# Kernel tuning notes

Hardware: AMD Instinct MI355X
Metric: run time of the kernel (lower is better)

The kernel has to match this reference:

```python
import jax, jax.numpy as jnp
import numpy as np

NEG_INF_SCALE = -1e9


def setup_inputs() -> dict:
    key = jax.random.key(0)
    ks = jax.random.split(key, 8)
    B, T, M, D = 64, 1024, 256, 1024
    query = jax.random.normal(ks[0], (B, 1, M), dtype=jnp.float32)
    keys = jax.random.normal(ks[1], (B, T, M), dtype=jnp.float32)
    values = jax.random.normal(ks[2], (B, T, D), dtype=jnp.float32)
    mask = jax.random.randint(ks[3], (B, 1, T), 0, 2).astype(jnp.float32)
    # MLP params (scaled like torch default init ~ 1/sqrt(fan_in))
    W1 = jax.random.normal(ks[4], (4 * M, D), dtype=jnp.float32) / np.sqrt(4 * M)
    b1 = jnp.zeros((D,), dtype=jnp.float32)
    W2 = jax.random.normal(ks[5], (D, D), dtype=jnp.float32) / np.sqrt(D)
    b2 = jnp.zeros((D,), dtype=jnp.float32)
    w_score = jax.random.normal(ks[6], (D, 1), dtype=jnp.float32) / np.sqrt(D)
    b_score = jnp.zeros((1,), dtype=jnp.float32)
    return {"query": query, "keys": keys, "values": values, "mask": mask,
            "W1": W1, "b1": b1, "W2": W2, "b2": b2,
            "w_score": w_score, "b_score": b_score}


def reference(query, keys, values, mask, W1, b1, W2, b2, w_score, b_score):
    # query: [B,1,M] broadcast against keys: [B,T,M]
    q = jnp.broadcast_to(query, keys.shape)
    att_input = jnp.concatenate([q, keys, q - keys, q * keys], axis=-1)  # [B,T,4M]
    h = jax.nn.relu(att_input @ W1 + b1)   # [B,T,D]
    h = jax.nn.relu(h @ W2 + b2)           # [B,T,D]
    score = h @ w_score + b_score          # [B,T,1]
    logits = jnp.swapaxes(score, 1, 2)     # [B,1,T]
    logits = logits + mask * NEG_INF_SCALE
    attn = jax.nn.softmax(logits, axis=-1)  # [B,1,T]
    out = jnp.matmul(attn, values)          # [B,1,D]
    return out
```

## Files before the change

kernel.cpp:

```cpp
#include <hip/hip_runtime.h>

#define DEV __device__ __forceinline__

typedef __attribute__((ext_vector_type(4))) float f32x4;
typedef __attribute__((ext_vector_type(8))) short short8;
typedef __attribute__((ext_vector_type(4))) short s16x4;
typedef __attribute__((ext_vector_type(4))) float f32x4v;

DEV short f2bf(float f) {
  union { float f; unsigned u; } v; v.f = f;
  unsigned r = (v.u + 0x7FFFu + ((v.u >> 16) & 1u)) >> 16;
  return (short)r;
}

DEV void gload16(const void* g, void* l) {
  __builtin_amdgcn_global_load_lds(
      (const __attribute__((address_space(1))) void*)g,
      (__attribute__((address_space(3))) void*)l, 16, 0, 0);
}

#define BAR() __builtin_amdgcn_s_barrier()
#define LGKMW(n)                                              \
  {                                                           \
    asm volatile("s_waitcnt lgkmcnt(" #n ")" ::: "memory");   \
    __builtin_amdgcn_sched_barrier(0);                        \
  }
#define VMW(n)                                                \
  {                                                           \
    asm volatile("s_waitcnt vmcnt(" #n ")" ::: "memory");     \
    __builtin_amdgcn_sched_barrier(0);                        \
  }


__global__ __launch_bounds__(256) void k_prep_all(
    const float* __restrict__ keys, const float* __restrict__ w2,
    const float* __restrict__ w1, const float* __restrict__ query,
    const float* __restrict__ b1, short* __restrict__ keysb,
    short* __restrict__ w2f, short* __restrict__ wktf,
    float* __restrict__ biasb) {
  __shared__ __align__(16) char smem[45056];
  const int bid = blockIdx.x;
  const int tid = threadIdx.x;

  if (bid < 256) {
    short (*tile)[64][72] = (short (*)[64][72])(smem);
    float (*qlds)[256] = (float (*)[256])(smem + 36864);
    float (*redm)[64][4] = (float (*)[64][4])(smem + 40960);
    const int r = bid;
    const int bg = r & 15, d0g = r >> 4, d0 = d0g * 64;
    const int d = tid & 63, mq = tid >> 6;

    for (int idx = tid; idx < 1024; idx += 256)
      qlds[idx >> 8][idx & 255] = query[(bg * 4 + (idx >> 8)) * 256 + (idx & 255)];
    __syncthreads();

    float bacc[4] = {0.f, 0.f, 0.f, 0.f};
    const int l = tid & 63, cgl = tid >> 6;

    for (int mc = 0; mc < 4; ++mc) {
#pragma unroll 4
      for (int i = 0; i < 16; ++i) {
        int ml = i * 4 + mq;
        int m = mc * 64 + ml;
        float wa = w1[(size_t)m * 1024 + d0 + d];
        float wb = w1[(size_t)(256 + m) * 1024 + d0 + d];
        float wc = w1[(size_t)(512 + m) * 1024 + d0 + d];
        float wd = w1[(size_t)(768 + m) * 1024 + d0 + d];
        float bc = wb - wc, ac = wa + wc;
#pragma unroll
        for (int bb = 0; bb < 4; ++bb) {
          float qv = qlds[bb][m];
          tile[bb][d][ml] = f2bf(bc + qv * wd);
          bacc[bb] += qv * ac;
        }
      }
      __syncthreads();
#pragma unroll
      for (int bb = 0; bb < 4; ++bb) {
        short* ob = wktf + (size_t)(bg * 4 + bb) * 262144;
#pragma unroll
        for (int kh = 0; kh < 2; ++kh) {
          short8 v = *(const short8*)&tile[bb][cgl * 16 + (l & 15)]
                                          [kh * 32 + (l >> 4) * 8];
          *(short8*)&ob[((size_t)((mc * 2 + kh) * 64 + d0g * 4 + cgl)) * 512 + l * 8] = v;
        }
      }
      __syncthreads();
    }

    redm[0][d][mq] = bacc[0];
    redm[1][d][mq] = bacc[1];
    redm[2][d][mq] = bacc[2];
    redm[3][d][mq] = bacc[3];
    __syncthreads();
    const int bb = tid >> 6, dd = tid & 63;
    biasb[(bg * 4 + bb) * 1024 + d0 + dd] =
        redm[bb][dd][0] + redm[bb][dd][1] + redm[bb][dd][2] + redm[bb][dd][3] +
        b1[d0 + dd];
  } else if (bid < 512) {
    float (*tile)[65] = (float (*)[65])(smem);
    const int r = bid - 256;
    const int kt = r & 15, n0 = (r >> 4) * 64;
    const int a = tid & 63, q = tid >> 6;
#pragma unroll
    for (int i = 0; i < 16; ++i) {
      int kk = i * 4 + q;
      tile[kk][a] = w2[(size_t)(kt * 64 + kk) * 1024 + n0 + a];
    }
    __syncthreads();
    const int l = tid & 63, cgl = tid >> 6;
#pragma unroll
    for (int kh = 0; kh < 2; ++kh) {
      short8 v;
#pragma unroll
      for (int j = 0; j < 8; ++j)
        v[j] = f2bf(tile[kh * 32 + (l >> 4) * 8 + j][cgl * 16 + (l & 15)]);
      *(short8*)&w2f[((size_t)((kt * 2 + kh) * 64 + (n0 >> 4) + cgl)) * 512 + l * 8] = v;
    }
  } else {
    int i = ((bid - 512) * 256 + tid) * 8;
    f32x4v v0 = *(const f32x4v*)(keys + i);
    f32x4v v1 = *(const f32x4v*)(keys + i + 4);
    short8 s;
    s[0] = f2bf(v0[0]); s[1] = f2bf(v0[1]); s[2] = f2bf(v0[2]); s[3] = f2bf(v0[3]);
    s[4] = f2bf(v1[0]); s[5] = f2bf(v1[1]); s[6] = f2bf(v1[2]); s[7] = f2bf(v1[3]);
    *(short8*)(keysb + i) = s;
  }
}


template <int MODE>
__global__ __launch_bounds__(256, 2) void k_gemm(const short* __restrict__ A,
                                                 const short* __restrict__ Bf,
                                                 const float* __restrict__ bias,
                                                 const float* __restrict__ wscore,
                                                 short* __restrict__ hout,
                                                 float* __restrict__ spart) {
  __shared__ short lds[32768];
  constexpr int SK = (MODE == 1) ? 256 : 1024;
  constexpr int KT = (MODE == 1) ? 4 : 16;

  const int tid = threadIdx.x;
  const int bx = blockIdx.x;
  const int L = (bx & 7) * 256 + (bx >> 3);

  const short *Ab, *Bb;
  const float *biasp, *wsp = nullptr;
  short* houtp = nullptr;
  int rt, ct;
  if constexpr (MODE == 1) {
    const int b = L >> 5;
    rt = (L >> 2) & 7; ct = L & 3;
    Ab = A + ((size_t)(b * 1024 + rt * 128)) * 256;
    Bb = Bf + (size_t)b * 262144;
    biasp = bias + b * 1024 + ct * 256;
    houtp = hout + ((size_t)(b * 1024 + rt * 128)) * 1024 + ct * 256;
  } else {
    rt = L >> 2; ct = L & 3;
    Ab = A + (size_t)rt * 128 * 1024;
    Bb = Bf;
    biasp = bias + ct * 256;
    wsp = wscore + ct * 256;
  }

  int gA[4], dA[4];
#pragma unroll
  for (int j = 0; j < 4; ++j) {
    int s = tid + j * 256, row = s >> 3, kc = (s & 7) ^ (row & 7);
    gA[j] = row * SK + kc * 8;
    dA[j] = s * 8;
  }
  auto STAGE = [&](int kt) {
    const int bb = (kt & 3) * 8192;
#pragma unroll
    for (int j = 0; j < 4; ++j) gload16(Ab + gA[j] + kt * 64, &lds[bb + dA[j]]);
  };

  const int lane = tid & 63, l15 = lane & 15, l4 = lane >> 4, wc = tid >> 6;
  const int afo0 = l15 * 64 + ((l4 ^ (l15 & 7)) * 8);
  const int afo1 = l15 * 64 + (((4 + l4) ^ (l15 & 7)) * 8);

  f32x4 acc[8][4];
#pragma unroll
  for (int m = 0; m < 8; ++m)
#pragma unroll
    for (int n = 0; n < 4; ++n) acc[m][n] = f32x4{0.f, 0.f, 0.f, 0.f};
  short8 bf[2][4][2];
  short8 af[8];

#define LOADB(kt, BK_)                                                          \
  _Pragma("unroll") for (int n_ = 0; n_ < 4; ++n_) {                            \
    _Pragma("unroll") for (int kh_ = 0; kh_ < 2; ++kh_) {                       \
      bf[BK_][n_][kh_] = *(const short8*)(Bb +                                  \
          ((size_t)(((kt) * 2 + kh_) * 64 + ct * 16 + n_ * 4 + wc) << 9) +      \
          lane * 8);                                                            \
    }                                                                           \
  }

  STAGE(0); LOADB(0, 0);
  STAGE(1); LOADB(1, 1);
  VMW(12);
  BAR();

#pragma unroll
  for (int t = 0; t < KT; ++t) {
    const int bb = (t & 3) * 8192;
#pragma unroll
    for (int m = 0; m < 8; ++m) af[m] = *(const short8*)&lds[bb + afo0 + m * 1024];
    LGKMW(0);
    __builtin_amdgcn_s_setprio(1);
#pragma unroll
    for (int m = 0; m < 8; ++m)
#pragma unroll
      for (int n = 0; n < 4; ++n)
        acc[m][n] = __builtin_amdgcn_mfma_f32_16x16x32_bf16(bf[t & 1][n][0], af[m],
                                                            acc[m][n], 0, 0, 0);
    __builtin_amdgcn_s_setprio(0);
#pragma unroll
    for (int m = 0; m < 8; ++m) af[m] = *(const short8*)&lds[bb + afo1 + m * 1024];
    if (t + 2 < KT) STAGE(t + 2);
    LGKMW(0);
    __builtin_amdgcn_s_setprio(1);
#pragma unroll
    for (int m = 0; m < 8; ++m)
#pragma unroll
      for (int n = 0; n < 4; ++n)
        acc[m][n] = __builtin_amdgcn_mfma_f32_16x16x32_bf16(bf[t & 1][n][1], af[m],
                                                            acc[m][n], 0, 0, 0);
    __builtin_amdgcn_s_setprio(0);
    if (t + 2 < KT) {
      LOADB(t + 2, (t & 1));
      VMW(12);
    } else {
      VMW(0);
    }
    BAR();
  }
#undef LOADB

  if constexpr (MODE == 1) {
    float bv[4][4];
#pragma unroll
    for (int n = 0; n < 4; ++n)
#pragma unroll
      for (int r2 = 0; r2 < 4; ++r2)
        bv[n][r2] = biasp[n * 64 + wc * 16 + l4 * 4 + r2];
#pragma unroll
    for (int m = 0; m < 8; ++m) {
      int row = m * 16 + l15;
#pragma unroll
      for (int n = 0; n < 4; ++n) {
        s16x4 pk;
#pragma unroll
        for (int r2 = 0; r2 < 4; ++r2)
          pk[r2] = f2bf(fmaxf(acc[m][n][r2] + bv[n][r2], 0.f));
        *(s16x4*)&houtp[(size_t)row * 1024 + n * 64 + wc * 16 + l4 * 4] = pk;
      }
    }
  } else {
    float bv[4][4], wv[4][4];
#pragma unroll
    for (int n = 0; n < 4; ++n)
#pragma unroll
      for (int r2 = 0; r2 < 4; ++r2) {
        int c = n * 64 + wc * 16 + l4 * 4 + r2;
        bv[n][r2] = biasp[c];
        wv[n][r2] = wsp[c];
      }
    float* so = spart + ((size_t)(ct * 4 + wc) << 16) + rt * 128;
#pragma unroll
    for (int m = 0; m < 8; ++m) {
      float s = 0.f;
#pragma unroll
      for (int n = 0; n < 4; ++n)
#pragma unroll
        for (int r2 = 0; r2 < 4; ++r2)
          s += fmaxf(acc[m][n][r2] + bv[n][r2], 0.f) * wv[n][r2];
      s += __shfl_xor(s, 16);
      s += __shfl_xor(s, 32);
      if (lane < 16) so[m * 16 + l15] = s;
    }
  }
}

__global__ __launch_bounds__(256) void k_out(const float* __restrict__ spart,
                                             const float* __restrict__ mask,
                                             const float* __restrict__ bscore,
                                             const float* __restrict__ values,
                                             float* __restrict__ part) {
  const int b = blockIdx.x >> 3, ts = blockIdx.x & 7;
  const int tid = threadIdx.x;
  __shared__ float sm[1024];
  __shared__ float red[8];
  const float bs = bscore[0];
  float lmax = -3.0e38f;
  for (int t = tid; t < 1024; t += 256) {
    float s = bs;
#pragma unroll
    for (int c = 0; c < 16; ++c) s += spart[(size_t)c * 65536 + b * 1024 + t];
    float lg = s + mask[b * 1024 + t] * (-1e9f);
    sm[t] = lg;
    lmax = fmaxf(lmax, lg);
  }
  for (int o = 32; o; o >>= 1) lmax = fmaxf(lmax, __shfl_xor(lmax, o));
  const int wid = tid >> 6, lane = tid & 63;
  if (lane == 0) red[wid] = lmax;
  __syncthreads();
  float bmax = fmaxf(fmaxf(red[0], red[1]), fmaxf(red[2], red[3]));
  float lsum = 0.f;
  for (int t = tid; t < 1024; t += 256) {
    float e = __expf(sm[t] - bmax);
    sm[t] = e;
    lsum += e;
  }
  for (int o = 32; o; o >>= 1) lsum += __shfl_xor(lsum, o);
  __syncthreads();
  if (lane == 0) red[wid] = lsum;
  __syncthreads();
  const float inv = 1.0f / (red[0] + red[1] + red[2] + red[3]);

  const float* vb = values + ((size_t)b * 1024 + ts * 128) * 1024 + tid * 4;
  f32x4 acc = {0.f, 0.f, 0.f, 0.f};
#pragma unroll 8
  for (int t = 0; t < 128; ++t) {
    f32x4v v = *(const f32x4v*)(vb + (size_t)t * 1024);
    float a = sm[ts * 128 + t] * inv;
    acc[0] += a * v[0]; acc[1] += a * v[1]; acc[2] += a * v[2]; acc[3] += a * v[3];
  }
  *(f32x4*)(part + ((size_t)(b * 8 + ts)) * 1024 + tid * 4) = acc;
}

__global__ __launch_bounds__(256) void k_red(const float* __restrict__ part,
                                             float* __restrict__ out) {
  const int b = blockIdx.x;
  const int c4 = threadIdx.x * 4;
  f32x4 s = {0.f, 0.f, 0.f, 0.f};
#pragma unroll
  for (int ts = 0; ts < 8; ++ts) {
    f32x4v v = *(const f32x4v*)(part + ((size_t)(b * 8 + ts)) * 1024 + c4);
    s[0] += v[0]; s[1] += v[1]; s[2] += v[2]; s[3] += v[3];
  }
  *(f32x4*)(out + b * 1024 + c4) = s;
}


extern "C" void kernel_launch(void* const* d_in, const int* in_sizes, int n_in,
                              void* d_out, int out_size, void* d_ws, size_t ws_size,
                              hipStream_t stream) {
  const float* query  = (const float*)d_in[0];
  const float* keys   = (const float*)d_in[1];
  const float* values = (const float*)d_in[2];
  const float* mask   = (const float*)d_in[3];
  const float* W1     = (const float*)d_in[4];
  const float* b1     = (const float*)d_in[5];
  const float* W2     = (const float*)d_in[6];
  const float* b2     = (const float*)d_in[7];
  const float* wscore = (const float*)d_in[8];
  const float* bscore = (const float*)d_in[9];
  float* out = (float*)d_out;

  char* ws = (char*)d_ws;
  short* keysb = (short*)(ws);
  short* wktf  = (short*)(ws + 33554432ull);
  short* w2f   = (short*)(ws + 67108864ull);
  float* biasb = (float*)(ws + 69206016ull);
  short* h1    = (short*)(ws + 69468160ull);
  float* spart = (float*)(ws + 203685888ull);
  float* part  = (float*)(ws + 207880192ull);

  k_prep_all<<<8704, 256, 0, stream>>>(keys, W2, W1, query, b1,
                                       keysb, w2f, wktf, biasb);

  k_gemm<1><<<2048, 256, 0, stream>>>(keysb, wktf, biasb, nullptr, h1, nullptr);
  k_gemm<2><<<2048, 256, 0, stream>>>(h1, w2f, b2, wscore, nullptr, spart);

  k_out<<<512, 256, 0, stream>>>(spart, mask, bscore, values, part);
  k_red<<<64, 256, 0, stream>>>(part, out);
}
```

Measured before the change: 253.7 us.

## Halve GEMM row tile to 64 with 3-stage LDS ring and just-in-time B loads

Shrinks the per-block M tile from 128 to 64 rows, doubling the grid to 4096 blocks, and cuts LDS to a 3-buffer ring of 64x64 tiles so three blocks can share a CU. B fragments are now loaded from global right before each k-half instead of being prefetched two steps ahead, which lowers register pressure. The column mapping per wave changes so each wave owns a contiguous 64-column strip, and the epilogues are updated to match. Each B fragment is now reused across half as many rows, which raises B traffic and exposes more global-load latency in exchange for higher occupancy.

After: 269.6 us. +6.3%, slower.

```diff
diff --git a/kernel.cpp b/kernel.cpp
--- a/kernel.cpp
+++ b/kernel.cpp
@@ -130,107 +130,106 @@
 
 
 template <int MODE>
-__global__ __launch_bounds__(256, 2) void k_gemm(const short* __restrict__ A,
+__global__ __launch_bounds__(256, 3) void k_gemm(const short* __restrict__ A,
                                                  const short* __restrict__ Bf,
                                                  const float* __restrict__ bias,
                                                  const float* __restrict__ wscore,
                                                  short* __restrict__ hout,
                                                  float* __restrict__ spart) {
-  __shared__ short lds[32768];
+  __shared__ short lds[12288];
   constexpr int SK = (MODE == 1) ? 256 : 1024;
   constexpr int KT = (MODE == 1) ? 4 : 16;
 
   const int tid = threadIdx.x;
   const int bx = blockIdx.x;
-  const int L = (bx & 7) * 256 + (bx >> 3);
+  const int L = (bx & 7) * 512 + (bx >> 3);
 
   const short *Ab, *Bb;
   const float *biasp, *wsp = nullptr;
   short* houtp = nullptr;
   int rt, ct;
   if constexpr (MODE == 1) {
-    const int b = L >> 5;
-    rt = (L >> 2) & 7; ct = L & 3;
-    Ab = A + ((size_t)(b * 1024 + rt * 128)) * 256;
+    const int b = L >> 6;
+    rt = (L >> 2) & 15; ct = L & 3;
+    Ab = A + ((size_t)(b * 1024 + rt * 64)) * 256;
     Bb = Bf + (size_t)b * 262144;
     biasp = bias + b * 1024 + ct * 256;
-    houtp = hout + ((size_t)(b * 1024 + rt * 128)) * 1024 + ct * 256;
+    houtp = hout + ((size_t)(b * 1024 + rt * 64)) * 1024 + ct * 256;
   } else {
     rt = L >> 2; ct = L & 3;
-    Ab = A + (size_t)rt * 128 * 1024;
+    Ab = A + (size_t)rt * 64 * 1024;
     Bb = Bf;
     biasp = bias + ct * 256;
     wsp = wscore + ct * 256;
   }
 
-  int gA[4], dA[4];
-#pragma unroll
-  for (int j = 0; j < 4; ++j) {
+  int gA[2], dA[2];
+#pragma unroll
+  for (int j = 0; j < 2; ++j) {
     int s = tid + j * 256, row = s >> 3, kc = (s & 7) ^ (row & 7);
     gA[j] = row * SK + kc * 8;
     dA[j] = s * 8;
   }
   auto STAGE = [&](int kt) {
-    const int bb = (kt & 3) * 8192;
-#pragma unroll
-    for (int j = 0; j < 4; ++j) gload16(Ab + gA[j] + kt * 64, &lds[bb + dA[j]]);
+    const int bb = (kt % 3) * 4096;
+#pragma unroll
+    for (int j = 0; j < 2; ++j) gload16(Ab + gA[j] + kt * 64, &lds[bb + dA[j]]);
   };
 
   const int lane = tid & 63, l15 = lane & 15, l4 = lane >> 4, wc = tid >> 6;
   const int afo0 = l15 * 64 + ((l4 ^ (l15 & 7)) * 8);
   const int afo1 = l15 * 64 + (((4 + l4) ^ (l15 & 7)) * 8);
 
-  f32x4 acc[8][4];
-#pragma unroll
-  for (int m = 0; m < 8; ++m)
+  f32x4 acc[4][4];
+#pragma unroll
+  for (int m = 0; m < 4; ++m)
 #pragma unroll
     for (int n = 0; n < 4; ++n) acc[m][n] = f32x4{0.f, 0.f, 0.f, 0.f};
-  short8 bf[2][4][2];
-  short8 af[8];
-
-#define LOADB(kt, BK_)                                                          \
+  short8 bf[4];
+  short8 af[4];
+
+#define LOADB(kt, kh_)                                                          \
   _Pragma("unroll") for (int n_ = 0; n_ < 4; ++n_) {                            \
-    _Pragma("unroll") for (int kh_ = 0; kh_ < 2; ++kh_) {                       \
-      bf[BK_][n_][kh_] = *(const short8*)(Bb +                                  \
-          ((size_t)(((kt) * 2 + kh_) * 64 + ct * 16 + n_ * 4 + wc) << 9) +      \
-          lane * 8);                                                            \
-    }                                                                           \
-  }
-
-  STAGE(0); LOADB(0, 0);
-  STAGE(1); LOADB(1, 1);
-  VMW(12);
+    bf[n_] = *(const short8*)(Bb +                                              \
+        ((size_t)(((kt) * 2 + (kh_)) * 64 + ct * 16 + wc * 4 + n_) << 9) +      \
+        lane * 8);                                                              \
+  }
+
+  STAGE(0);
+  STAGE(1);
+  VMW(2);
   BAR();
 
 #pragma unroll
   for (int t = 0; t < KT; ++t) {
-    const int bb = (t & 3) * 8192;
-#pragma unroll
-    for (int m = 0; m < 8; ++m) af[m] = *(const short8*)&lds[bb + afo0 + m * 1024];
+    const int bb = (t % 3) * 4096;
+    LOADB(t, 0);
+#pragma unroll
+    for (int m = 0; m < 4; ++m) af[m] = *(const short8*)&lds[bb + afo0 + m * 1024];
     LGKMW(0);
     __builtin_amdgcn_s_setprio(1);
 #pragma unroll
-    for (int m = 0; m < 8; ++m)
+    for (int m = 0; m < 4; ++m)
 #pragma unroll
       for (int n = 0; n < 4; ++n)
-        acc[m][n] = __builtin_amdgcn_mfma_f32_16x16x32_bf16(bf[t & 1][n][0], af[m],
+        acc[m][n] = __builtin_amdgcn_mfma_f32_16x16x32_bf16(bf[n], af[m],
                                                             acc[m][n], 0, 0, 0);
     __builtin_amdgcn_s_setprio(0);
-#pragma unroll
-    for (int m = 0; m < 8; ++m) af[m] = *(const short8*)&lds[bb + afo1 + m * 1024];
+    LOADB(t, 1);
     if (t + 2 < KT) STAGE(t + 2);
+#pragma unroll
+    for (int m = 0; m < 4; ++m) af[m] = *(const short8*)&lds[bb + afo1 + m * 1024];
     LGKMW(0);
     __builtin_amdgcn_s_setprio(1);
 #pragma unroll
-    for (int m = 0; m < 8; ++m)
+    for (int m = 0; m < 4; ++m)
 #pragma unroll
       for (int n = 0; n < 4; ++n)
-        acc[m][n] = __builtin_amdgcn_mfma_f32_16x16x32_bf16(bf[t & 1][n][1], af[m],
+        acc[m][n] = __builtin_amdgcn_mfma_f32_16x16x32_bf16(bf[n], af[m],
                                                             acc[m][n], 0, 0, 0);
     __builtin_amdgcn_s_setprio(0);
     if (t + 2 < KT) {
-      LOADB(t + 2, (t & 1));
-      VMW(12);
+      VMW(2);
     } else {
       VMW(0);
     }
@@ -244,9 +243,9 @@
     for (int n = 0; n < 4; ++n)
 #pragma unroll
       for (int r2 = 0; r2 < 4; ++r2)
-        bv[n][r2] = biasp[n * 64 + wc * 16 + l4 * 4 + r2];
-#pragma unroll
-    for (int m = 0; m < 8; ++m) {
+        bv[n][r2] = biasp[wc * 64 + n * 16 + l4 * 4 + r2];
+#pragma unroll
+    for (int m = 0; m < 4; ++m) {
       int row = m * 16 + l15;
 #pragma unroll
       for (int n = 0; n < 4; ++n) {
@@ -254,7 +253,7 @@
 #pragma unroll
         for (int r2 = 0; r2 < 4; ++r2)
           pk[r2] = f2bf(fmaxf(acc[m][n][r2] + bv[n][r2], 0.f));
-        *(s16x4*)&houtp[(size_t)row * 1024 + n * 64 + wc * 16 + l4 * 4] = pk;
+        *(s16x4*)&houtp[(size_t)row * 1024 + wc * 64 + n * 16 + l4 * 4] = pk;
       }
     }
   } else {
@@ -263,13 +262,13 @@
     for (int n = 0; n < 4; ++n)
 #pragma unroll
       for (int r2 = 0; r2 < 4; ++r2) {
-        int c = n * 64 + wc * 16 + l4 * 4 + r2;
+        int c = wc * 64 + n * 16 + l4 * 4 + r2;
         bv[n][r2] = biasp[c];
         wv[n][r2] = wsp[c];
       }
-    float* so = spart + ((size_t)(ct * 4 + wc) << 16) + rt * 128;
-#pragma unroll
-    for (int m = 0; m < 8; ++m) {
+    float* so = spart + ((size_t)(ct * 4 + wc) << 16) + rt * 64;
+#pragma unroll
+    for (int m = 0; m < 4; ++m) {
       float s = 0.f;
 #pragma unroll
       for (int n = 0; n < 4; ++n)
@@ -371,8 +370,8 @@
   k_prep_all<<<8704, 256, 0, stream>>>(keys, W2, W1, query, b1,
                                        keysb, w2f, wktf, biasb);
 
-  k_gemm<1><<<2048, 256, 0, stream>>>(keysb, wktf, biasb, nullptr, h1, nullptr);
-  k_gemm<2><<<2048, 256, 0, stream>>>(h1, w2f, b2, wscore, nullptr, spart);
+  k_gemm<1><<<4096, 256, 0, stream>>>(keysb, wktf, biasb, nullptr, h1, nullptr);
+  k_gemm<2><<<4096, 256, 0, stream>>>(h1, w2f, b2, wscore, nullptr, spart);
 
   k_out<<<512, 256, 0, stream>>>(spart, mask, bscore, values, part);
   k_red<<<64, 256, 0, stream>>>(part, out);
```
